# Optimization experiments

Hardware: AMD Instinct MI355X
Metric: run time of the kernel (lower is better)

The kernel has to match this reference:

```python
import jax, jax.numpy as jnp
import numpy as np

ROI_SIZE = 7
SPATIAL_SCALE = 1.0 / 16.0
CHUNK = 16  # rois processed per lax.map step to bound the masked-max intermediate


def roi_pool(x, indices_and_rois):
    """Caffe-style RoI max pooling. x: [N,C,H,W]; indices_and_rois: [R,5]=(idx,x1,y1,x2,y2)."""
    N, C, H, W = x.shape
    P = ROI_SIZE
    hi = jnp.arange(H, dtype=x.dtype)
    wi = jnp.arange(W, dtype=x.dtype)
    p = jnp.arange(P, dtype=x.dtype)

    def pool_one(r5):
        idx = r5[0].astype(jnp.int32)
        xmin, ymin, xmax, ymax = r5[1], r5[2], r5[3], r5[4]
        sw = jnp.round(xmin * SPATIAL_SCALE)
        sh = jnp.round(ymin * SPATIAL_SCALE)
        ew = jnp.round(xmax * SPATIAL_SCALE)
        eh = jnp.round(ymax * SPATIAL_SCALE)
        bw = jnp.maximum(ew - sw + 1.0, 1.0) / P  # bin width in feature cells
        bh = jnp.maximum(eh - sh + 1.0, 1.0) / P
        wstart = jnp.clip(jnp.floor(p * bw) + sw, 0.0, float(W))
        wend = jnp.clip(jnp.ceil((p + 1.0) * bw) + sw, 0.0, float(W))
        hstart = jnp.clip(jnp.floor(p * bh) + sh, 0.0, float(H))
        hend = jnp.clip(jnp.ceil((p + 1.0) * bh) + sh, 0.0, float(H))
        colmask = (wi[None, :] >= wstart[:, None]) & (wi[None, :] < wend[:, None])  # [P,W]
        rowmask = (hi[None, :] >= hstart[:, None]) & (hi[None, :] < hend[:, None])  # [P,H]
        img = x[idx]  # [C,H,W] gather of the roi's image
        neg = jnp.asarray(-jnp.inf, x.dtype)
        # max over columns within each column-bin, then over rows within each row-bin
        m1 = jnp.max(jnp.where(colmask[None, None, :, :], img[:, :, None, :], neg), axis=-1)  # [C,H,P]
        m2 = jnp.max(jnp.where(rowmask[None, :, :, None], m1[:, None, :, :], neg), axis=2)  # [C,P,P]
        return jnp.where(jnp.isfinite(m2), m2, jnp.zeros((), x.dtype))  # empty bins -> 0

    R = indices_and_rois.shape[0]
    chunks = indices_and_rois.reshape(R // CHUNK, CHUNK, 5)
    pooled = jax.lax.map(jax.vmap(pool_one), chunks)  # [R//CHUNK, CHUNK, C, P, P]
    return pooled.reshape(R, C, P, P)


def setup_inputs() -> dict:
    key = jax.random.key(0)
    ks = jax.random.split(key, 8)
    N, C, H, W = 4, 512, 50, 50  # 800x800 image, VGG16 stride 16
    R, n_class = 512, 21
    x = jax.random.normal(ks[0], (N, C, H, W), jnp.float32)
    yx1 = jax.random.uniform(ks[1], (R, 2), jnp.float32, 0.0, 700.0)
    wh = jax.random.uniform(ks[2], (R, 2), jnp.float32, 32.0, 128.0)
    rois = jnp.concatenate([yx1, jnp.minimum(yx1 + wh, 799.0)], axis=1)  # (y1,x1,y2,x2)
    roi_indices = jax.random.randint(ks[3], (R,), 0, N)
    din = C * ROI_SIZE * ROI_SIZE
    W1 = jax.random.normal(ks[4], (din, 4096), jnp.float32) * 0.01
    b1 = jnp.zeros((4096,), jnp.float32)
    W2 = jax.random.normal(ks[5], (4096, 4096), jnp.float32) * 0.01
    b2 = jnp.zeros((4096,), jnp.float32)
    Wc = jax.random.normal(ks[6], (4096, n_class * 4), jnp.float32) * 0.001
    bc = jnp.zeros((n_class * 4,), jnp.float32)
    Ws = jax.random.normal(ks[7], (4096, n_class), jnp.float32) * 0.01
    bs = jnp.zeros((n_class,), jnp.float32)
    return {"x": x, "rois": rois, "roi_indices": roi_indices, "W1": W1, "b1": b1,
            "W2": W2, "b2": b2, "Wc": Wc, "bc": bc, "Ws": Ws, "bs": bs}


def reference(x, rois, roi_indices, W1, b1, W2, b2, Wc, bc, Ws, bs):
    # concat index + boxes, then reorder (idx,y1,x1,y2,x2) -> (idx,x1,y1,x2,y2)
    ir = jnp.concatenate([roi_indices[:, None].astype(jnp.float32), rois], axis=1)
    ir = ir[:, jnp.array([0, 2, 1, 4, 3])]
    pool = roi_pool(x, ir)  # [R, C, 7, 7]
    flat = pool.reshape(pool.shape[0], -1)  # [R, 25088]
    fc6 = jax.nn.relu(flat @ W1 + b1)
    fc7 = jax.nn.relu(fc6 @ W2 + b2)
    roi_cls_locs = fc7 @ Wc + bc  # [R, n_class*4]
    roi_scores = fc7 @ Ws + bs  # [R, n_class]
    return (roi_cls_locs, roi_scores)
```

## Files before the change

### kernel.cpp

```cpp
#include <hip/hip_runtime.h>
#include <math.h>

typedef __attribute__((ext_vector_type(8))) short short8;
typedef __attribute__((ext_vector_type(4))) short s16x4;
typedef __attribute__((ext_vector_type(4))) float f32x4;
typedef __attribute__((ext_vector_type(4))) unsigned u32x4;

#define R_ROIS 512
#define CCH 512
#define HH 50
#define WW 50
#define PPOOL 7
#define KDIM (CCH * PPOOL * PPOOL)
#define NH 4096
#define ZSPLIT 8
#define NHEAD 105
#define POOL_SLICES 16

#define BARRIER_NO_VMDRAIN()                              \
  do {                                                    \
    asm volatile("s_waitcnt lgkmcnt(0)" ::: "memory");    \
    __builtin_amdgcn_s_barrier();                         \
  } while (0)

__device__ __forceinline__ short f2bf(float f) {
  unsigned u = __builtin_bit_cast(unsigned, f);
  u += 0x7FFFu + ((u >> 16) & 1u);
  return (short)(u >> 16);
}
__device__ __forceinline__ float bf2f(short s) {
  unsigned u = ((unsigned)(unsigned short)s) << 16;
  return __builtin_bit_cast(float, u);
}
__device__ __forceinline__ unsigned cvtpk(float lo, float hi) {
  unsigned r;
  asm("v_cvt_pk_bf16_f32 %0, %1, %2" : "=v"(r) : "v"(lo), "v"(hi));
  return r;
}

__global__ __launch_bounds__(256) void roi_pool_kernel(
    const float* __restrict__ x, const float* __restrict__ rois,
    const int* __restrict__ ridx, short* __restrict__ A) {
  __shared__ int hs[PPOOL], he[PPOOL], wss[PPOOL], wee[PPOOL];
  __shared__ int sidx;
  const int r = blockIdx.x;
  if (threadIdx.x == 0) {
    float ymin = rois[r * 4 + 0], xmin = rois[r * 4 + 1];
    float ymax = rois[r * 4 + 2], xmax = rois[r * 4 + 3];
    float sw = rintf(xmin * 0.0625f);
    float sh = rintf(ymin * 0.0625f);
    float ew = rintf(xmax * 0.0625f);
    float eh = rintf(ymax * 0.0625f);
    float bw = fmaxf(ew - sw + 1.0f, 1.0f) * (1.0f / 7.0f);
    float bh = fmaxf(eh - sh + 1.0f, 1.0f) * (1.0f / 7.0f);
    for (int p = 0; p < PPOOL; ++p) {
      wss[p] = (int)fminf(fmaxf(floorf(p * bw) + sw, 0.0f), 50.0f);
      wee[p] = (int)fminf(fmaxf(ceilf((p + 1) * bw) + sw, 0.0f), 50.0f);
      hs[p]  = (int)fminf(fmaxf(floorf(p * bh) + sh, 0.0f), 50.0f);
      he[p]  = (int)fminf(fmaxf(ceilf((p + 1) * bh) + sh, 0.0f), 50.0f);
    }
    sidx = ridx[r];
  }
  __syncthreads();
  const float* xb = x + (size_t)sidx * CCH * HH * WW;
  const int obeg = blockIdx.y * (KDIM / POOL_SLICES);
  const int oend = obeg + KDIM / POOL_SLICES;
  for (int o = obeg + threadIdx.x; o < oend; o += 256) {
    int c = o / 49;
    int pq = o - c * 49;
    int ph = pq / 7, pw = pq - ph * 7;
    const float* xc = xb + (size_t)c * (HH * WW);
    int h0 = hs[ph], h1 = he[ph], w0 = wss[pw], w1 = wee[pw];
    float mv = -INFINITY;
    for (int h = h0; h < h1; ++h) {
      const float* xr = xc + h * WW;
      for (int w = w0; w < w1; ++w) mv = fmaxf(mv, xr[w]);
    }
    A[(size_t)r * KDIM + o] = f2bf((h1 > h0 && w1 > w0) ? mv : 0.0f);
  }
}

__global__ __launch_bounds__(512, 2) void gemm_splitk_kernel(
    const short* __restrict__ A, const float* __restrict__ B,
    short* __restrict__ part, int M, int N, int K, int Ks, int nblk) {
  __shared__ __align__(16) char As[2][256 * 64];
  __shared__ __align__(16) char Bs[2][256 * 64];
  const int bid = blockIdx.x;
  const int vid = (bid & 7) * (nblk >> 3) + (bid >> 3);
  const int mb = vid & 1;
  const int nb = (vid >> 1) & 15;
  const int zb = vid >> 5;
  const int m0 = mb * 256, n0 = nb * 256;
  const int kbeg = zb * Ks;
  const int S = Ks >> 5;
  const int t = threadIdx.x;
  const int lane = t & 63, wid = t >> 6;
  const int wm = wid >> 2, wn = wid & 3;
  const int lr = lane & 15, kc = lane >> 4;
  const int ar = t >> 1, ah = t & 1;
  const int bn = t & 255, bko = t >> 8;

  const short* aptrA = A + (size_t)(m0 + ar) * K + ah * 16;
  const float* bbase = B + n0 + bn;

  const int awz0 = (ar * 64 + ah * 32) ^ ((ar & 7) << 4);
  const int awz1 = awz0 ^ 16;
  const int bwz0 = (bn * 64 + bko * 32) ^ ((bn & 7) << 4);
  const int bwz1 = bwz0 ^ 16;
  const int aoff = (wm * 8192 + lr * 64 + kc * 16) ^ ((lr & 7) << 4);
  const int boff = (wn * 4096 + lr * 64 + kc * 16) ^ ((lr & 7) << 4);

  f32x4 acc[8][4] = {};
  short8 aA0, aA1, aB0, aB1;
  float bA[16], bB[16];

  auto LOADT = [&](int k0, short8& r0, short8& r1, float* br) {
    r0 = *(const short8*)(aptrA + k0);
    r1 = *(const short8*)(aptrA + k0 + 8);
    const float* bp = bbase + (size_t)(k0 + bko * 16) * N;
    #pragma unroll
    for (int j = 0; j < 16; ++j) br[j] = bp[(size_t)j * N];
  };
  auto WRITET = [&](int buf, const short8& r0, const short8& r1, const float* br) {
    *(short8*)(As[buf] + awz0) = r0;
    *(short8*)(As[buf] + awz1) = r1;
    u32x4 w0, w1;
    w0[0] = cvtpk(br[0], br[1]);   w0[1] = cvtpk(br[2], br[3]);
    w0[2] = cvtpk(br[4], br[5]);   w0[3] = cvtpk(br[6], br[7]);
    w1[0] = cvtpk(br[8], br[9]);   w1[1] = cvtpk(br[10], br[11]);
    w1[2] = cvtpk(br[12], br[13]); w1[3] = cvtpk(br[14], br[15]);
    *(u32x4*)(Bs[buf] + bwz0) = w0;
    *(u32x4*)(Bs[buf] + bwz1) = w1;
  };
  auto COMPUTE = [&](int buf) {
    short8 b[4];
    #pragma unroll
    for (int n = 0; n < 4; ++n)
      b[n] = *(const short8*)(Bs[buf] + boff + n * 1024);
    #pragma unroll
    for (int m = 0; m < 8; ++m) {
      short8 a = *(const short8*)(As[buf] + aoff + m * 1024);
      #pragma unroll
      for (int n = 0; n < 4; ++n)
        acc[m][n] = __builtin_amdgcn_mfma_f32_16x16x32_bf16(a, b[n], acc[m][n], 0, 0, 0);
    }
  };

  LOADT(kbeg, aA0, aA1, bA);
  WRITET(0, aA0, aA1, bA);
  LOADT(kbeg + 32, aB0, aB1, bB);
  BARRIER_NO_VMDRAIN();

  int cur = 0;
  for (int i = 0; i < S; i += 2) {
    if (i + 2 < S) LOADT(kbeg + (i + 2) * 32, aA0, aA1, bA);
    COMPUTE(cur);
    WRITET(cur ^ 1, aB0, aB1, bB);
    BARRIER_NO_VMDRAIN();
    cur ^= 1;
    if (i + 3 < S) LOADT(kbeg + (i + 3) * 32, aB0, aB1, bB);
    COMPUTE(cur);
    if (i + 2 < S) {
      WRITET(cur ^ 1, aA0, aA1, bA);
      BARRIER_NO_VMDRAIN();
      cur ^= 1;
    }
  }

  short* pz = part + (size_t)zb * M * N;
  #pragma unroll
  for (int m = 0; m < 8; ++m) {
    #pragma unroll
    for (int n = 0; n < 4; ++n) {
      int col = n0 + wn * 64 + n * 16 + lr;
      #pragma unroll
      for (int j = 0; j < 4; ++j) {
        int row = m0 + wm * 128 + m * 16 + kc * 4 + j;
        pz[(size_t)row * N + col] = f2bf(acc[m][n][j]);
      }
    }
  }
}

__global__ __launch_bounds__(256) void reduce_relu_kernel(
    const short* __restrict__ part, const float* __restrict__ bias,
    short* __restrict__ out, int MN, int N) {
  int i = (blockIdx.x * 256 + threadIdx.x) * 4;
  if (i >= MN) return;
  const float4 b = *(const float4*)(bias + (i & (N - 1)));
  float s0 = 0.0f, s1 = 0.0f, s2 = 0.0f, s3 = 0.0f;
  #pragma unroll
  for (int z = 0; z < ZSPLIT; ++z) {
    s16x4 p = *(const s16x4*)(part + (size_t)z * MN + i);
    s0 += bf2f(p.x); s1 += bf2f(p.y); s2 += bf2f(p.z); s3 += bf2f(p.w);
  }
  s16x4 o;
  o.x = f2bf(fmaxf(s0 + b.x, 0.0f));
  o.y = f2bf(fmaxf(s1 + b.y, 0.0f));
  o.z = f2bf(fmaxf(s2 + b.z, 0.0f));
  o.w = f2bf(fmaxf(s3 + b.w, 0.0f));
  *(s16x4*)(out + i) = o;
}

__global__ __launch_bounds__(256) void pack_head_w_kernel(
    const float* __restrict__ Wc, const float* __restrict__ Wsv,
    short* __restrict__ Wt) {
  const int n = blockIdx.x;
  for (int k = threadIdx.x; k < NH; k += 256) {
    float v = 0.0f;
    if (n < 84) v = Wc[(size_t)k * 84 + n];
    else if (n < NHEAD) v = Wsv[(size_t)k * 21 + (n - 84)];
    Wt[(size_t)n * NH + k] = f2bf(v);
  }
}

__global__ __launch_bounds__(256, 2) void gemm_head_kernel(
    const short* __restrict__ A, const short* __restrict__ Bt,
    float* __restrict__ part2) {
  __shared__ __align__(16) char As[2][128 * 64];
  __shared__ __align__(16) char Bs[2][128 * 64];
  const int m0 = blockIdx.x * 128;
  const int zb = blockIdx.y;
  const int kbeg = zb * (NH / ZSPLIT), kend = kbeg + NH / ZSPLIT;
  const int t = threadIdx.x;
  const int lane = t & 63, wid = t >> 6;
  const int wm = wid >> 1, wn = wid & 1;
  const int lr = lane & 15, kc = lane >> 4;
  const int sr = t >> 2, seg = t & 3;

  const short* aptr0 = A + (size_t)(m0 + sr) * NH + seg * 8;
  const short* aptr1 = aptr0 + (size_t)64 * NH;
  const short* bptr0 = Bt + (size_t)sr * NH + seg * 8;
  const short* bptr1 = bptr0 + (size_t)64 * NH;

  const int wz0 = (sr * 64 + seg * 16) ^ ((sr & 7) << 4);
  const int wz1 = wz0 + 4096;
  const int aoff = (wm * 4096 + lr * 64 + kc * 16) ^ ((lr & 7) << 4);
  const int boff = (wn * 4096 + lr * 64 + kc * 16) ^ ((lr & 7) << 4);

  f32x4 acc[4][4] = {};
  short8 a_r0, a_r1, b_r0, b_r1;

  auto LOADT = [&](int k0) {
    a_r0 = *(const short8*)(aptr0 + k0);
    a_r1 = *(const short8*)(aptr1 + k0);
    b_r0 = *(const short8*)(bptr0 + k0);
    b_r1 = *(const short8*)(bptr1 + k0);
  };
  auto WRITET = [&](int buf) {
    *(short8*)(As[buf] + wz0) = a_r0;
    *(short8*)(As[buf] + wz1) = a_r1;
    *(short8*)(Bs[buf] + wz0) = b_r0;
    *(short8*)(Bs[buf] + wz1) = b_r1;
  };
  auto COMPUTE = [&](int buf) {
    short8 a[4], b[4];
    #pragma unroll
    for (int m = 0; m < 4; ++m)
      a[m] = *(const short8*)(As[buf] + aoff + m * 1024);
    #pragma unroll
    for (int n = 0; n < 4; ++n)
      b[n] = *(const short8*)(Bs[buf] + boff + n * 1024);
    #pragma unroll
    for (int m = 0; m < 4; ++m)
      #pragma unroll
      for (int n = 0; n < 4; ++n)
        acc[m][n] = __builtin_amdgcn_mfma_f32_16x16x32_bf16(a[m], b[n], acc[m][n], 0, 0, 0);
  };

  LOADT(kbeg);
  WRITET(0);
  BARRIER_NO_VMDRAIN();

  int cur = 0;
  for (int k0 = kbeg + 32; k0 <= kend; k0 += 32) {
    bool more = (k0 < kend);
    if (more) LOADT(k0);
    COMPUTE(cur);
    if (more) {
      WRITET(cur ^ 1);
      BARRIER_NO_VMDRAIN();
      cur ^= 1;
    }
  }

  float* pz = part2 + (size_t)zb * R_ROIS * 128;
  #pragma unroll
  for (int m = 0; m < 4; ++m) {
    #pragma unroll
    for (int n = 0; n < 4; ++n) {
      int col = wn * 64 + n * 16 + lr;
      #pragma unroll
      for (int j = 0; j < 4; ++j) {
        int row = m0 + wm * 64 + m * 16 + kc * 4 + j;
        pz[(size_t)row * 128 + col] = acc[m][n][j];
      }
    }
  }
}

__global__ __launch_bounds__(128) void reduce_head_kernel(
    const float* __restrict__ part2, const float* __restrict__ bc,
    const float* __restrict__ bs, float* __restrict__ out) {
  const int r = blockIdx.x, c = threadIdx.x;
  if (c >= NHEAD) return;
  float s = 0.0f;
  #pragma unroll
  for (int z = 0; z < ZSPLIT; ++z)
    s += part2[(size_t)z * R_ROIS * 128 + (size_t)r * 128 + c];
  if (c < 84)
    out[(size_t)r * 84 + c] = s + bc[c];
  else
    out[(size_t)R_ROIS * 84 + (size_t)r * 21 + (c - 84)] = s + bs[c - 84];
}

extern "C" void kernel_launch(void* const* d_in, const int* in_sizes, int n_in,
                              void* d_out, int out_size, void* d_ws, size_t ws_size,
                              hipStream_t stream) {
  const float* x    = (const float*)d_in[0];
  const float* rois = (const float*)d_in[1];
  const int*   ridx = (const int*)d_in[2];
  const float* W1   = (const float*)d_in[3];
  const float* b1   = (const float*)d_in[4];
  const float* W2   = (const float*)d_in[5];
  const float* b2   = (const float*)d_in[6];
  const float* Wc   = (const float*)d_in[7];
  const float* bc   = (const float*)d_in[8];
  const float* Wsv  = (const float*)d_in[9];
  const float* bs   = (const float*)d_in[10];

  const int MN = R_ROIS * NH;
  short* A     = (short*)d_ws;
  short* fc6   = A + (size_t)R_ROIS * KDIM;
  short* fc7   = fc6 + (size_t)MN;
  short* part  = fc7 + (size_t)MN;
  float* part2 = (float*)(part + (size_t)ZSPLIT * MN);
  short* Wt    = (short*)(part2 + (size_t)ZSPLIT * R_ROIS * 128);

  roi_pool_kernel<<<dim3(R_ROIS, POOL_SLICES), 256, 0, stream>>>(x, rois, ridx, A);
  pack_head_w_kernel<<<128, 256, 0, stream>>>(Wc, Wsv, Wt);

  gemm_splitk_kernel<<<256, 512, 0, stream>>>(A, W1, part, R_ROIS, NH, KDIM,
                                              KDIM / ZSPLIT, 256);
  reduce_relu_kernel<<<MN / 4 / 256, 256, 0, stream>>>(part, b1, fc6, MN, NH);

  gemm_splitk_kernel<<<256, 512, 0, stream>>>(fc6, W2, part, R_ROIS, NH, NH,
                                              NH / ZSPLIT, 256);
  reduce_relu_kernel<<<MN / 4 / 256, 256, 0, stream>>>(part, b2, fc7, MN, NH);

  gemm_head_kernel<<<dim3(4, ZSPLIT), 256, 0, stream>>>(fc7, Wt, part2);
  reduce_head_kernel<<<R_ROIS, 128, 0, stream>>>(part2, bc, bs, (float*)d_out);
}
```

Measured before the change: 273.0 us.

## Double GEMM K-tile to 64 with single register-staged prefetch

```diff
diff --git a/kernel.cpp b/kernel.cpp
--- a/kernel.cpp
+++ b/kernel.cpp
@@ -83,16 +83,15 @@
 __global__ __launch_bounds__(512, 2) void gemm_splitk_kernel(
     const short* __restrict__ A, const float* __restrict__ B,
     short* __restrict__ part, int M, int N, int K, int Ks, int nblk) {
-  __shared__ __align__(16) char As[2][256 * 64];
-  __shared__ __align__(16) char Bs[2][256 * 64];
+  __shared__ __align__(16) char As[2][256 * 128];
+  __shared__ __align__(16) char Bs[2][256 * 128];
   const int bid = blockIdx.x;
   const int vid = (bid & 7) * (nblk >> 3) + (bid >> 3);
   const int mb = vid & 1;
   const int nb = (vid >> 1) & 15;
   const int zb = vid >> 5;
   const int m0 = mb * 256, n0 = nb * 256;
-  const int kbeg = zb * Ks;
-  const int S = Ks >> 5;
+  const int kbeg = zb * Ks, kend = kbeg + Ks;
   const int t = threadIdx.x;
   const int lane = t & 63, wid = t >> 6;
   const int wm = wid >> 2, wn = wid & 3;
@@ -100,68 +99,74 @@
   const int ar = t >> 1, ah = t & 1;
   const int bn = t & 255, bko = t >> 8;
 
-  const short* aptrA = A + (size_t)(m0 + ar) * K + ah * 16;
+  const short* aptrA = A + (size_t)(m0 + ar) * K + ah * 32;
   const float* bbase = B + n0 + bn;
 
-  const int awz0 = (ar * 64 + ah * 32) ^ ((ar & 7) << 4);
-  const int awz1 = awz0 ^ 16;
-  const int bwz0 = (bn * 64 + bko * 32) ^ ((bn & 7) << 4);
-  const int bwz1 = bwz0 ^ 16;
-  const int aoff = (wm * 8192 + lr * 64 + kc * 16) ^ ((lr & 7) << 4);
-  const int boff = (wn * 4096 + lr * 64 + kc * 16) ^ ((lr & 7) << 4);
+  int awz[4], bwz[4];
+  #pragma unroll
+  for (int j = 0; j < 4; ++j) {
+    awz[j] = ar * 128 + (((ah * 4 + j) ^ (ar & 7)) << 4);
+    bwz[j] = bn * 128 + (((bko * 4 + j) ^ (bn & 7)) << 4);
+  }
+  const int aoff = (wm * 128 + lr) * 128 + ((kc ^ (lr & 7)) << 4);
+  const int boff = (wn * 64 + lr) * 128 + ((kc ^ (lr & 7)) << 4);
 
   f32x4 acc[8][4] = {};
-  short8 aA0, aA1, aB0, aB1;
-  float bA[16], bB[16];
-
-  auto LOADT = [&](int k0, short8& r0, short8& r1, float* br) {
-    r0 = *(const short8*)(aptrA + k0);
-    r1 = *(const short8*)(aptrA + k0 + 8);
-    const float* bp = bbase + (size_t)(k0 + bko * 16) * N;
-    #pragma unroll
-    for (int j = 0; j < 16; ++j) br[j] = bp[(size_t)j * N];
-  };
-  auto WRITET = [&](int buf, const short8& r0, const short8& r1, const float* br) {
-    *(short8*)(As[buf] + awz0) = r0;
-    *(short8*)(As[buf] + awz1) = r1;
-    u32x4 w0, w1;
-    w0[0] = cvtpk(br[0], br[1]);   w0[1] = cvtpk(br[2], br[3]);
-    w0[2] = cvtpk(br[4], br[5]);   w0[3] = cvtpk(br[6], br[7]);
-    w1[0] = cvtpk(br[8], br[9]);   w1[1] = cvtpk(br[10], br[11]);
-    w1[2] = cvtpk(br[12], br[13]); w1[3] = cvtpk(br[14], br[15]);
-    *(u32x4*)(Bs[buf] + bwz0) = w0;
-    *(u32x4*)(Bs[buf] + bwz1) = w1;
+  short8 a_r0, a_r1, a_r2, a_r3;
+  float br[32];
+
+  auto LOADT = [&](int k0) {
+    a_r0 = *(const short8*)(aptrA + k0);
+    a_r1 = *(const short8*)(aptrA + k0 + 8);
+    a_r2 = *(const short8*)(aptrA + k0 + 16);
+    a_r3 = *(const short8*)(aptrA + k0 + 24);
+    const float* bp = bbase + (size_t)(k0 + bko * 32) * N;
+    #pragma unroll
+    for (int j = 0; j < 32; ++j) br[j] = bp[(size_t)j * N];
+  };
+  auto WRITET = [&](int buf) {
+    *(short8*)(As[buf] + awz[0]) = a_r0;
+    *(short8*)(As[buf] + awz[1]) = a_r1;
+    *(short8*)(As[buf] + awz[2]) = a_r2;
+    *(short8*)(As[buf] + awz[3]) = a_r3;
+    #pragma unroll
+    for (int j = 0; j < 4; ++j) {
+      u32x4 w;
+      w[0] = cvtpk(br[j * 8 + 0], br[j * 8 + 1]);
+      w[1] = cvtpk(br[j * 8 + 2], br[j * 8 + 3]);
+      w[2] = cvtpk(br[j * 8 + 4], br[j * 8 + 5]);
+      w[3] = cvtpk(br[j * 8 + 6], br[j * 8 + 7]);
+      *(u32x4*)(Bs[buf] + bwz[j]) = w;
+    }
   };
   auto COMPUTE = [&](int buf) {
-    short8 b[4];
-    #pragma unroll
-    for (int n = 0; n < 4; ++n)
-      b[n] = *(const short8*)(Bs[buf] + boff + n * 1024);
-    #pragma unroll
-    for (int m = 0; m < 8; ++m) {
-      short8 a = *(const short8*)(As[buf] + aoff + m * 1024);
+    #pragma unroll
+    for (int kk = 0; kk < 2; ++kk) {
+      short8 b[4];
       #pragma unroll
       for (int n = 0; n < 4; ++n)
-        acc[m][n] = __builtin_amdgcn_mfma_f32_16x16x32_bf16(a, b[n], acc[m][n], 0, 0, 0);
-    }
-  };
-
-  LOADT(kbeg, aA0, aA1, bA);
-  WRITET(0, aA0, aA1, bA);
-  LOADT(kbeg + 32, aB0, aB1, bB);
+        b[n] = *(const short8*)(Bs[buf] + ((boff + n * 2048) ^ (kk << 6)));
+      #pragma unroll
+      for (int m = 0; m < 8; ++m) {
+        short8 a = *(const short8*)(As[buf] + ((aoff + m * 2048) ^ (kk << 6)));
+        #pragma unroll
+        for (int n = 0; n < 4; ++n)
+          acc[m][n] = __builtin_amdgcn_mfma_f32_16x16x32_bf16(a, b[n], acc[m][n], 0, 0, 0);
+      }
+    }
+  };
+
+  LOADT(kbeg);
+  WRITET(0);
   BARRIER_NO_VMDRAIN();
 
   int cur = 0;
-  for (int i = 0; i < S; i += 2) {
-    if (i + 2 < S) LOADT(kbeg + (i + 2) * 32, aA0, aA1, bA);
+  for (int k0 = kbeg + 64; k0 <= kend; k0 += 64) {
+    bool more = (k0 < kend);
+    if (more) LOADT(k0);
     COMPUTE(cur);
-    WRITET(cur ^ 1, aB0, aB1, bB);
-    BARRIER_NO_VMDRAIN();
-    cur ^= 1;
-    if (i + 3 < S) LOADT(kbeg + (i + 3) * 32, aB0, aB1, bB);
-    COMPUTE(cur);
-    if (i + 2 < S) {
-      WRITET(cur ^ 1, aA0, aA1, bA);
+    if (more) {
+      WRITET(cur ^ 1);
       BARRIER_NO_VMDRAIN();
       cur ^= 1;
     }
```

Measured after the change: 270.1 us. No clear change (-1.1%).
